# Optimization experiments

Hardware: AMD Instinct MI355X
Metric: run time of the kernel (lower is better)

## Reference

```python
import jax, jax.numpy as jnp
import numpy as np

N_HEADS = 16
EMBED_DIM = 2048
BATCH, SEQ = 2, 2048


def setup_inputs() -> dict:
    key = jax.random.key(0)
    k1, k2, k3, k4, k5 = jax.random.split(key, 5)
    s_in = 1.0 / np.sqrt(EMBED_DIM)
    return {
        "x": jax.random.normal(k1, (BATCH, SEQ, EMBED_DIM), dtype=jnp.float32),
        "w_in": jax.random.normal(k2, (3 * EMBED_DIM, EMBED_DIM), dtype=jnp.float32) * s_in,
        "b_in": jax.random.normal(k3, (3 * EMBED_DIM,), dtype=jnp.float32) * 0.02,
        "w_out": jax.random.normal(k4, (EMBED_DIM, EMBED_DIM), dtype=jnp.float32) * s_in,
        "b_out": jax.random.normal(k5, (EMBED_DIM,), dtype=jnp.float32) * 0.02,
        "causal_mask": 1,
    }


def reference(x, w_in, b_in, w_out, b_out, causal_mask):
    b, l, e = x.shape
    h, d = N_HEADS, e // N_HEADS
    qkv = x @ w_in.T + b_in                      # [b, l, 3e]
    q, k, v = jnp.split(qkv, 3, axis=-1)
    # b l (h d) -> b h l d
    q = q.reshape(b, l, h, d).transpose(0, 2, 1, 3)
    k = k.reshape(b, l, h, d).transpose(0, 2, 1, 3)
    v = v.reshape(b, l, h, d).transpose(0, 2, 1, 3)
    scores = jnp.einsum("bhqd,bhkd->bhqk", q, k) / jnp.sqrt(jnp.float32(d))
    if causal_mask:
        tri = jnp.triu(jnp.ones((l, l), dtype=bool), k=1)  # True above diagonal
        scores = jnp.where(tri, -jnp.inf, scores)
    attn = jax.nn.softmax(scores, axis=-1)
    out = jnp.einsum("bhqk,bhkd->bhqd", attn, v)  # [b, h, l, d]
    out = out.transpose(0, 2, 1, 3).reshape(b, l, e)
    return out @ w_out.T + b_out
```

## Files before the change

### kernel.cpp

```cpp
#include <hip/hip_runtime.h>
#include <hip/hip_bf16.h>
#include <math.h>

typedef __attribute__((ext_vector_type(4))) float floatx4;
typedef __attribute__((ext_vector_type(16))) float floatx16;
typedef __attribute__((ext_vector_type(8))) __bf16 bf16x8;

__device__ __forceinline__ unsigned short f2bf(float f) {
    union { float f; unsigned int u; } v; v.f = f;
    unsigned int u = v.u;
    u += 0x7FFFu + ((u >> 16) & 1u);
    return (unsigned short)(u >> 16);
}

__device__ __forceinline__ unsigned int pkbf(float a, float b) {
    return (unsigned int)f2bf(a) | ((unsigned int)f2bf(b) << 16);
}

__device__ __forceinline__ void gl_lds16(const void* g, void* l) {
    __builtin_amdgcn_global_load_lds(
        (const __attribute__((address_space(1))) void*)g,
        (__attribute__((address_space(3))) void*)l, 16, 0, 0);
}

__global__ void cast_f32_bf16(const float* __restrict__ in,
                              unsigned short* __restrict__ out, int n) {
    int i = (blockIdx.x * blockDim.x + threadIdx.x) * 4;
    if (i + 4 <= n) {
        float4 f = *(const float4*)(in + i);
        ushort4 o;
        o.x = f2bf(f.x); o.y = f2bf(f.y); o.z = f2bf(f.z); o.w = f2bf(f.w);
        *(ushort4*)(out + i) = o;
    }
}

#define BM 128
#define BN 128
#define BK 32
#define GROUP_M 8

template<int MODE>
__global__ __launch_bounds__(256) void gemm_nt(
    const unsigned short* __restrict__ A,
    const unsigned short* __restrict__ B,
    const float* __restrict__ bias,
    float* __restrict__ Cf,
    unsigned short* __restrict__ q_ws,
    unsigned short* __restrict__ k_ws,
    unsigned short* __restrict__ vT_ws,
    int M, int N, int K)
{
    __shared__ unsigned short Asm[BM][BK];
    __shared__ unsigned short Bsm[BN][BK];

    const int id = blockIdx.x + gridDim.x * blockIdx.y;
    const int perGroup = gridDim.x * GROUP_M;
    const int group = id / perGroup;
    const int rem = id % perGroup;
    const int gh = min(GROUP_M, (int)gridDim.y - group * GROUP_M);
    const int by = group * GROUP_M + rem % gh;
    const int bx = rem / gh;

    const int m0 = by * BM, n0 = bx * BN;
    const int tid = threadIdx.x;
    const int lane = tid & 63, wid = tid >> 6;
    const int quad = lane >> 4, li = lane & 15;
    const int wy = wid >> 1, wx = wid & 1;

    const int lrow = lane >> 2;
    const int lcol = (lane & 3) * 8;

    floatx4 acc[4][4] = {};

    const int kTiles = K / BK;
    for (int kt = 0; kt < kTiles; ++kt) {
        const int k0 = kt * BK;
        #pragma unroll
        for (int c = 0; c < 2; ++c) {
            const int cidx = wid * 2 + c;
            const int row = cidx * 16 + lrow;
            gl_lds16(A + (size_t)(m0 + row) * K + k0 + lcol,
                     &Asm[0][0] + cidx * 512);
            gl_lds16(B + (size_t)(n0 + row) * K + k0 + lcol,
                     &Bsm[0][0] + cidx * 512);
        }
        __syncthreads();

        bf16x8 af[4], bfr[4];
        #pragma unroll
        for (int t = 0; t < 4; ++t) {
            af[t]  = *(const bf16x8*)(&Asm[wy * 64 + t * 16 + li][quad * 8]);
            bfr[t] = *(const bf16x8*)(&Bsm[wx * 64 + t * 16 + li][quad * 8]);
        }
        #pragma unroll
        for (int i = 0; i < 4; ++i)
            #pragma unroll
            for (int j = 0; j < 4; ++j)
                acc[i][j] = __builtin_amdgcn_mfma_f32_16x16x32_bf16(
                    af[i], bfr[j], acc[i][j], 0, 0, 0);
        __syncthreads();
    }

    if (MODE == 0) {
        #pragma unroll
        for (int i = 0; i < 4; ++i)
            #pragma unroll
            for (int j = 0; j < 4; ++j) {
                int col = wx * 64 + j * 16 + li;
                float bv = bias[n0 + col];
                #pragma unroll
                for (int r = 0; r < 4; ++r) {
                    int row = wy * 64 + i * 16 + quad * 4 + r;
                    Cf[(size_t)(m0 + row) * N + n0 + col] = acc[i][j][r] + bv;
                }
            }
    } else {
        const int which = bx >> 4;
        const int h = bx & 15;
        const int b = by >> 4;
        const int lbase = (by & 15) * BM;
        const size_t bh = (size_t)(b * 16 + h);
        #pragma unroll
        for (int i = 0; i < 4; ++i)
            #pragma unroll
            for (int j = 0; j < 4; ++j) {
                int col = wx * 64 + j * 16 + li;
                float bv = bias[n0 + col];
                #pragma unroll
                for (int r = 0; r < 4; ++r) {
                    int row = wy * 64 + i * 16 + quad * 4 + r;
                    int l = lbase + row;
                    unsigned short ob = f2bf(acc[i][j][r] + bv);
                    if (which == 0)      q_ws[(bh * 2048 + l) * 128 + col] = ob;
                    else if (which == 1) k_ws[(bh * 2048 + l) * 128 + col] = ob;
                    else                 vT_ws[(bh * 128 + col) * 2048 + l] = ob;
                }
            }
    }
}

#define AP 8
__global__ __launch_bounds__(256, 2) void attn_kernel(
    const unsigned short* __restrict__ q_ws,
    const unsigned short* __restrict__ k_ws,
    const unsigned short* __restrict__ vT_ws,
    unsigned short* __restrict__ aout,
    const int* __restrict__ causal_ptr)
{
    __shared__ unsigned short Ksm[128][128 + AP];
    __shared__ unsigned short Vsm[128][128 + AP];

    const int ord = blockIdx.x;
    int qt, bhid;
    if (ord < 256) { qt = ord >> 5;              bhid = ord & 31; }
    else           { qt = 15 - ((ord - 256) >> 5); bhid = ord & 31; }
    const int b = bhid >> 4, h = bhid & 15;

    const int tid = threadIdx.x;
    const int lane = tid & 63, w = tid >> 6;
    const int lq = lane & 31;
    const int half = lane >> 5;
    const size_t bh = (size_t)(b * 16 + h);
    const unsigned short* Qp = q_ws + bh * 2048 * 128;
    const unsigned short* Kp = k_ws + bh * 2048 * 128;
    const unsigned short* Vp = vT_ws + bh * 128 * 2048;
    const int causal = causal_ptr[0];
    const float scale = 0.08838834764831845f;

    const int qg = qt * 128 + w * 32 + lq;
    bf16x8 qf[8];
    #pragma unroll
    for (int s = 0; s < 8; ++s)
        qf[s] = *(const bf16x8*)(Qp + (size_t)qg * 128 + s * 16 + half * 8);

    floatx16 O[4] = {};
    float m_i = -INFINITY, l_i = 0.f;

    const int myEnd = causal ? qt : 15;
    for (int kt = 0; kt <= myEnd; ++kt) {
        #pragma unroll
        for (int c = 0; c < 8; ++c) {
            int chunk = c * 256 + tid;
            int row = chunk >> 4;
            int cc  = (chunk & 15) * 8;
            *(uint4*)(&Ksm[row][cc]) =
                *(const uint4*)(Kp + (size_t)(kt * 128 + row) * 128 + cc);
            *(uint4*)(&Vsm[row][cc]) =
                *(const uint4*)(Vp + (size_t)row * 2048 + kt * 128 + cc);
        }
        __syncthreads();

        floatx16 S[4] = {};
        #pragma unroll
        for (int ct = 0; ct < 4; ++ct)
            #pragma unroll
            for (int s = 0; s < 8; ++s) {
                bf16x8 kf = *(const bf16x8*)(&Ksm[ct * 32 + lq][s * 16 + half * 8]);
                S[ct] = __builtin_amdgcn_mfma_f32_32x32x16_bf16(kf, qf[s], S[ct], 0, 0, 0);
            }

        const bool diag = causal && (kt == qt);
        float mx = -INFINITY;
        #pragma unroll
        for (int ct = 0; ct < 4; ++ct)
            #pragma unroll
            for (int r = 0; r < 16; ++r) {
                float sv = S[ct][r] * scale;
                if (diag) {
                    int key = 32 * ct + (r & 3) + 8 * (r >> 2) + 4 * half;
                    if (kt * 128 + key > qg) sv = -INFINITY;
                }
                S[ct][r] = sv;
                mx = fmaxf(mx, sv);
            }
        mx = fmaxf(mx, __shfl_xor(mx, 32, 64));
        float m_new = fmaxf(m_i, mx);
        float m_use = (m_new == -INFINITY) ? 0.f : m_new;
        float alpha = __expf(m_i - m_use);

        float rs = 0.f;
        #pragma unroll
        for (int ct = 0; ct < 4; ++ct)
            #pragma unroll
            for (int r = 0; r < 16; ++r) {
                float p = __expf(S[ct][r] - m_use);
                S[ct][r] = p;
                rs += p;
            }
        rs += __shfl_xor(rs, 32, 64);
        l_i = l_i * alpha + rs;
        m_i = m_new;
        #pragma unroll
        for (int dt = 0; dt < 4; ++dt)
            #pragma unroll
            for (int r = 0; r < 16; ++r)
                O[dt][r] *= alpha;

        bf16x8 pfr[8];
        #pragma unroll
        for (int ct = 0; ct < 4; ++ct)
            #pragma unroll
            for (int h2 = 0; h2 < 2; ++h2) {
                int base = 8 * h2;
                unsigned int pk0 = pkbf(S[ct][base + 0], S[ct][base + 1]);
                unsigned int pk1 = pkbf(S[ct][base + 2], S[ct][base + 3]);
                unsigned int pk2 = pkbf(S[ct][base + 4], S[ct][base + 5]);
                unsigned int pk3 = pkbf(S[ct][base + 6], S[ct][base + 7]);
                unsigned int x0 = __shfl_xor((int)pk0, 32, 64);
                unsigned int x1 = __shfl_xor((int)pk1, 32, 64);
                unsigned int x2 = __shfl_xor((int)pk2, 32, 64);
                unsigned int x3 = __shfl_xor((int)pk3, 32, 64);
                union { unsigned int u[4]; bf16x8 v; } fr;
                fr.u[0] = half ? x2 : pk0;
                fr.u[1] = half ? x3 : pk1;
                fr.u[2] = half ? pk2 : x0;
                fr.u[3] = half ? pk3 : x1;
                pfr[ct * 2 + h2] = fr.v;
            }

        #pragma unroll
        for (int dt = 0; dt < 4; ++dt)
            #pragma unroll
            for (int s = 0; s < 8; ++s) {
                bf16x8 vf = *(const bf16x8*)(&Vsm[dt * 32 + lq][s * 16 + half * 8]);
                O[dt] = __builtin_amdgcn_mfma_f32_32x32x16_bf16(vf, pfr[s], O[dt], 0, 0, 0);
            }
        __syncthreads();
    }

    const float invl = 1.0f / l_i;
    #pragma unroll
    for (int dt = 0; dt < 4; ++dt)
        #pragma unroll
        for (int g = 0; g < 4; ++g) {
            int dbase = dt * 32 + g * 8 + half * 4;
            ushort4 o4;
            o4.x = f2bf(O[dt][g * 4 + 0] * invl);
            o4.y = f2bf(O[dt][g * 4 + 1] * invl);
            o4.z = f2bf(O[dt][g * 4 + 2] * invl);
            o4.w = f2bf(O[dt][g * 4 + 3] * invl);
            *(ushort4*)(&Ksm[w * 32 + lq][dbase]) = o4;
        }
    __syncthreads();
    #pragma unroll
    for (int c = 0; c < 8; ++c) {
        int chunk = c * 256 + tid;
        int row = chunk >> 4;
        int dc = (chunk & 15) * 8;
        uint4 v = *(const uint4*)(&Ksm[row][dc]);
        *(uint4*)(aout + ((size_t)b * 2048 + qt * 128 + row) * 2048 + h * 128 + dc) = v;
    }
}

extern "C" void kernel_launch(void* const* d_in, const int* in_sizes, int n_in,
                              void* d_out, int out_size, void* d_ws, size_t ws_size,
                              hipStream_t stream) {
    const float* x     = (const float*)d_in[0];
    const float* w_in  = (const float*)d_in[1];
    const float* b_in  = (const float*)d_in[2];
    const float* w_out = (const float*)d_in[3];
    const float* b_out = (const float*)d_in[4];
    const int* causal  = (const int*)d_in[5];

    char* ws = (char*)d_ws;
    unsigned short* xb    = (unsigned short*)ws; ws += (size_t)4096 * 2048 * 2;
    unsigned short* wb    = (unsigned short*)ws; ws += (size_t)6144 * 2048 * 2;
    unsigned short* wob   = (unsigned short*)ws; ws += (size_t)2048 * 2048 * 2;
    unsigned short* q_ws  = (unsigned short*)ws; ws += (size_t)32 * 2048 * 128 * 2;
    unsigned short* k_ws  = (unsigned short*)ws; ws += (size_t)32 * 2048 * 128 * 2;
    unsigned short* vT_ws = (unsigned short*)ws; ws += (size_t)32 * 2048 * 128 * 2;
    unsigned short* aout  = (unsigned short*)ws; ws += (size_t)4096 * 2048 * 2;

    cast_f32_bf16<<<8192, 256, 0, stream>>>(x, xb, 4096 * 2048);
    cast_f32_bf16<<<12288, 256, 0, stream>>>(w_in, wb, 6144 * 2048);
    cast_f32_bf16<<<4096, 256, 0, stream>>>(w_out, wob, 2048 * 2048);

    gemm_nt<1><<<dim3(48, 32), 256, 0, stream>>>(
        xb, wb, b_in, nullptr, q_ws, k_ws, vT_ws, 4096, 6144, 2048);

    attn_kernel<<<512, 256, 0, stream>>>(
        q_ws, k_ws, vT_ws, aout, causal);

    gemm_nt<0><<<dim3(16, 32), 256, 0, stream>>>(
        aout, wob, b_out, (float*)d_out, nullptr, nullptr, nullptr,
        4096, 2048, 2048);
}
```

Baseline: 434.4 us.

## Replace GEMM with 256x256 double-buffered 8-wave pipelined kernel with swizzled LDS

Replaces the simple 128x128x32 GEMM, which synchronized on every K step, with a 256x256 tile, BK=64 kernel using 512 threads. It double-buffers A/B tiles in 128KB of dynamic LDS, issues global->LDS loads interleaved with MFMA phases, and waits on explicit vmcnt counts. LDS addresses are XOR-swizzled to avoid bank conflicts, MFMA blocks are raised with setprio, and workgroups are remapped across XCDs. The V-transpose store is vectorized to ushort4. This adds complexity and tight manual synchronization. The output projection launches only 128 workgroups, which may underfill the GPU.

```diff
diff --git a/kernel.cpp b/kernel.cpp
--- a/kernel.cpp
+++ b/kernel.cpp
@@ -34,13 +34,43 @@
     }
 }
 
-#define BM 128
-#define BN 128
-#define BK 32
-#define GROUP_M 8
+
+#define VMCNT(n) asm volatile("s_waitcnt vmcnt(" #n ")" ::: "memory")
+#define BARF()   do { __builtin_amdgcn_s_barrier(); asm volatile("" ::: "memory"); } while (0)
+
+#define STAGE_A(bsel, tt, h) do { \
+    const unsigned short* _s = Ab + (size_t)((h) * 128 + rstage) * K + (tt) * 64 + scol; \
+    char* _d = bufc + (bsel) * 65536 + (h) * 16384 + wid * 1024; \
+    gl_lds16(_s, _d); \
+    gl_lds16(_s + (size_t)64 * K, _d + 8192); \
+} while (0)
+
+#define STAGE_B(bsel, tt, h) do { \
+    const unsigned short* _s = Bb + (size_t)((h) * 128 + rstage) * K + (tt) * 64 + scol; \
+    char* _d = bufc + (bsel) * 65536 + 32768 + (h) * 16384 + wid * 1024; \
+    gl_lds16(_s, _d); \
+    gl_lds16(_s + (size_t)64 * K, _d + 8192); \
+} while (0)
+
+#define RDA(base, ii, kse) (*(const bf16x8*)((base) + (ii) * 2048 + rdoffA + (kse)))
+#define RDB(base, jj, kse) (*(const bf16x8*)((base) + (jj) * 2048 + rdoffB + (kse)))
+
+#define MFMA_Q(iofs, jofs, BV) do { \
+    __builtin_amdgcn_s_setprio(1); \
+    _Pragma("unroll") \
+    for (int ii = 0; ii < 4; ++ii) { \
+        _Pragma("unroll") \
+        for (int jj = 0; jj < 2; ++jj) { \
+            acc[(iofs) + ii][(jofs) + jj] = __builtin_amdgcn_mfma_f32_16x16x32_bf16( \
+                aF[ii * 2 + 0], BV[jj * 2 + 0], acc[(iofs) + ii][(jofs) + jj], 0, 0, 0); \
+            acc[(iofs) + ii][(jofs) + jj] = __builtin_amdgcn_mfma_f32_16x16x32_bf16( \
+                aF[ii * 2 + 1], BV[jj * 2 + 1], acc[(iofs) + ii][(jofs) + jj], 0, 0, 0); \
+        } } \
+    __builtin_amdgcn_s_setprio(0); \
+} while (0)
 
 template<int MODE>
-__global__ __launch_bounds__(256) void gemm_nt(
+__global__ __launch_bounds__(512, 2) void gemm8p(
     const unsigned short* __restrict__ A,
     const unsigned short* __restrict__ B,
     const float* __restrict__ bias,
@@ -50,90 +80,146 @@
     unsigned short* __restrict__ vT_ws,
     int M, int N, int K)
 {
-    __shared__ unsigned short Asm[BM][BK];
-    __shared__ unsigned short Bsm[BN][BK];
-
-    const int id = blockIdx.x + gridDim.x * blockIdx.y;
-    const int perGroup = gridDim.x * GROUP_M;
-    const int group = id / perGroup;
-    const int rem = id % perGroup;
-    const int gh = min(GROUP_M, (int)gridDim.y - group * GROUP_M);
-    const int by = group * GROUP_M + rem % gh;
-    const int bx = rem / gh;
-
-    const int m0 = by * BM, n0 = bx * BN;
+    extern __shared__ char ldsc[];
+    char* const bufc = ldsc;
+
+    const int nby = M >> 8;
+    const int nwg = gridDim.x;
+    const int qq = nwg >> 3;
+    const int wg = (blockIdx.x & 7) * qq + (blockIdx.x >> 3);
+    const int by = wg % nby, bx = wg / nby;
+    const int m0 = by << 8, n0 = bx << 8;
+
     const int tid = threadIdx.x;
     const int lane = tid & 63, wid = tid >> 6;
-    const int quad = lane >> 4, li = lane & 15;
-    const int wy = wid >> 1, wx = wid & 1;
-
-    const int lrow = lane >> 2;
-    const int lcol = (lane & 3) * 8;
-
-    floatx4 acc[4][4] = {};
-
-    const int kTiles = K / BK;
-    for (int kt = 0; kt < kTiles; ++kt) {
-        const int k0 = kt * BK;
-        #pragma unroll
-        for (int c = 0; c < 2; ++c) {
-            const int cidx = wid * 2 + c;
-            const int row = cidx * 16 + lrow;
-            gl_lds16(A + (size_t)(m0 + row) * K + k0 + lcol,
-                     &Asm[0][0] + cidx * 512);
-            gl_lds16(B + (size_t)(n0 + row) * K + k0 + lcol,
-                     &Bsm[0][0] + cidx * 512);
-        }
-        __syncthreads();
-
-        bf16x8 af[4], bfr[4];
-        #pragma unroll
-        for (int t = 0; t < 4; ++t) {
-            af[t]  = *(const bf16x8*)(&Asm[wy * 64 + t * 16 + li][quad * 8]);
-            bfr[t] = *(const bf16x8*)(&Bsm[wx * 64 + t * 16 + li][quad * 8]);
-        }
-        #pragma unroll
-        for (int i = 0; i < 4; ++i)
-            #pragma unroll
-            for (int j = 0; j < 4; ++j)
-                acc[i][j] = __builtin_amdgcn_mfma_f32_16x16x32_bf16(
-                    af[i], bfr[j], acc[i][j], 0, 0, 0);
-        __syncthreads();
+    const int li = lane & 15, quad = lane >> 4;
+    const int wr = wid >> 2, wc = wid & 3;
+
+    const int rstage = tid >> 3;
+    const int scol = (((tid & 7) ^ ((tid >> 3) & 7)) << 3);
+    const unsigned short* Ab = A + (size_t)m0 * K;
+    const unsigned short* Bb = B + (size_t)n0 * K;
+
+    const int swz = (lane & 7) << 4;
+    const int ks0 = ((quad << 4)     ) ^ swz;
+    const int ks1 = ((quad << 4) + 64) ^ swz;
+    const int rdoffA = li * 128;
+    const int rdoffB = li * 128 + ((wc & 1) << 13);
+
+    const char* rdA0 = bufc + wr * 16384;
+    const char* rdB0 = bufc + 32768 + (wc >> 1) * 16384;
+    const char* rdA1 = rdA0 + 65536;
+    const char* rdB1 = rdB0 + 65536;
+
+    floatx4 acc[8][4] = {};
+    bf16x8 aF[8], bL[4], bH[4];
+
+    const int KTn = K >> 6;
+
+    STAGE_A(0, 0, 0); STAGE_A(0, 0, 1); STAGE_B(0, 0, 0); STAGE_B(0, 0, 1);
+    STAGE_B(1, 1, 0); STAGE_B(1, 1, 1); STAGE_A(1, 1, 0);
+    VMCNT(6);
+    BARF();
+
+    for (int t = 0; t < KTn; t += 2) {
+        const bool pf = (t + 2 < KTn);
+
+        #pragma unroll
+        for (int ii = 0; ii < 4; ++ii) { aF[ii*2+0] = RDA(rdA0, ii, ks0); aF[ii*2+1] = RDA(rdA0, ii, ks1); }
+        #pragma unroll
+        for (int jj = 0; jj < 2; ++jj) { bL[jj*2+0] = RDB(rdB0, jj, ks0); bL[jj*2+1] = RDB(rdB0, jj, ks1); }
+        STAGE_A(1, t + 1, 1);
+        BARF();
+        MFMA_Q(0, 0, bL);
+        BARF();
+
+        #pragma unroll
+        for (int jj = 0; jj < 2; ++jj) { bH[jj*2+0] = RDB(rdB0, 2 + jj, ks0); bH[jj*2+1] = RDB(rdB0, 2 + jj, ks1); }
+        BARF();
+        MFMA_Q(0, 2, bH);
+        BARF();
+
+        #pragma unroll
+        for (int ii = 0; ii < 4; ++ii) { aF[ii*2+0] = RDA(rdA0, 4 + ii, ks0); aF[ii*2+1] = RDA(rdA0, 4 + ii, ks1); }
+        if (pf) STAGE_B(0, t + 2, 0);
+        BARF();
+        MFMA_Q(4, 0, bL);
+        BARF();
+
+        if (pf) { STAGE_B(0, t + 2, 1); STAGE_A(0, t + 2, 0); }
+        BARF();
+        MFMA_Q(4, 2, bH);
+        if (pf) { VMCNT(6); } else { VMCNT(0); }
+        BARF();
+
+        #pragma unroll
+        for (int ii = 0; ii < 4; ++ii) { aF[ii*2+0] = RDA(rdA1, ii, ks0); aF[ii*2+1] = RDA(rdA1, ii, ks1); }
+        #pragma unroll
+        for (int jj = 0; jj < 2; ++jj) { bL[jj*2+0] = RDB(rdB1, jj, ks0); bL[jj*2+1] = RDB(rdB1, jj, ks1); }
+        if (pf) STAGE_A(0, t + 2, 1);
+        BARF();
+        MFMA_Q(0, 0, bL);
+        BARF();
+
+        #pragma unroll
+        for (int jj = 0; jj < 2; ++jj) { bH[jj*2+0] = RDB(rdB1, 2 + jj, ks0); bH[jj*2+1] = RDB(rdB1, 2 + jj, ks1); }
+        BARF();
+        MFMA_Q(0, 2, bH);
+        BARF();
+
+        #pragma unroll
+        for (int ii = 0; ii < 4; ++ii) { aF[ii*2+0] = RDA(rdA1, 4 + ii, ks0); aF[ii*2+1] = RDA(rdA1, 4 + ii, ks1); }
+        if (pf) STAGE_B(1, t + 3, 0);
+        BARF();
+        MFMA_Q(4, 0, bL);
+        BARF();
+
+        if (pf) { STAGE_B(1, t + 3, 1); STAGE_A(1, t + 3, 0); }
+        BARF();
+        MFMA_Q(4, 2, bH);
+        VMCNT(6);
+        BARF();
     }
 
+    const int colb = n0 + wc * 64;
+    const int rowb = m0 + wr * 128;
     if (MODE == 0) {
         #pragma unroll
-        for (int i = 0; i < 4; ++i)
-            #pragma unroll
-            for (int j = 0; j < 4; ++j) {
-                int col = wx * 64 + j * 16 + li;
-                float bv = bias[n0 + col];
+        for (int i2 = 0; i2 < 8; ++i2)
+            #pragma unroll
+            for (int j2 = 0; j2 < 4; ++j2) {
+                const int col = colb + j2 * 16 + li;
+                const float bv = bias[col];
                 #pragma unroll
                 for (int r = 0; r < 4; ++r) {
-                    int row = wy * 64 + i * 16 + quad * 4 + r;
-                    Cf[(size_t)(m0 + row) * N + n0 + col] = acc[i][j][r] + bv;
+                    const int row = rowb + i2 * 16 + quad * 4 + r;
+                    Cf[(size_t)row * N + col] = acc[i2][j2][r] + bv;
                 }
             }
     } else {
-        const int which = bx >> 4;
-        const int h = bx & 15;
-        const int b = by >> 4;
-        const int lbase = (by & 15) * BM;
-        const size_t bh = (size_t)(b * 16 + h);
-        #pragma unroll
-        for (int i = 0; i < 4; ++i)
-            #pragma unroll
-            for (int j = 0; j < 4; ++j) {
-                int col = wx * 64 + j * 16 + li;
-                float bv = bias[n0 + col];
-                #pragma unroll
-                for (int r = 0; r < 4; ++r) {
-                    int row = wy * 64 + i * 16 + quad * 4 + r;
-                    int l = lbase + row;
-                    unsigned short ob = f2bf(acc[i][j][r] + bv);
-                    if (which == 0)      q_ws[(bh * 2048 + l) * 128 + col] = ob;
-                    else if (which == 1) k_ws[(bh * 2048 + l) * 128 + col] = ob;
-                    else                 vT_ws[(bh * 128 + col) * 2048 + l] = ob;
+        const int bb = m0 >> 11;
+        const int which = n0 >> 11;
+        #pragma unroll
+        for (int i2 = 0; i2 < 8; ++i2)
+            #pragma unroll
+            for (int j2 = 0; j2 < 4; ++j2) {
+                const int ng = colb + j2 * 16 + li;
+                const float bv = bias[ng];
+                const int e = ng & 2047, hh = e >> 7, dd = e & 127;
+                const size_t bh = (size_t)(bb * 16 + hh);
+                const int l0 = (rowb + i2 * 16 + quad * 4) & 2047;
+                if (which == 2) {
+                    ushort4 o4;
+                    o4.x = f2bf(acc[i2][j2][0] + bv);
+                    o4.y = f2bf(acc[i2][j2][1] + bv);
+                    o4.z = f2bf(acc[i2][j2][2] + bv);
+                    o4.w = f2bf(acc[i2][j2][3] + bv);
+                    *(ushort4*)(vT_ws + (bh * 128 + dd) * 2048 + l0) = o4;
+                } else {
+                    unsigned short* dst = (which == 0) ? q_ws : k_ws;
+                    #pragma unroll
+                    for (int r = 0; r < 4; ++r)
+                        dst[(bh * 2048 + (l0 + r)) * 128 + dd] = f2bf(acc[i2][j2][r] + bv);
                 }
             }
     }
@@ -311,17 +397,28 @@
     unsigned short* vT_ws = (unsigned short*)ws; ws += (size_t)32 * 2048 * 128 * 2;
     unsigned short* aout  = (unsigned short*)ws; ws += (size_t)4096 * 2048 * 2;
 
+    static int once = []() {
+        auto* f0 = gemm8p<0>;
+        auto* f1 = gemm8p<1>;
+        hipFuncSetAttribute((const void*)f0,
+            hipFuncAttributeMaxDynamicSharedMemorySize, 131072);
+        hipFuncSetAttribute((const void*)f1,
+            hipFuncAttributeMaxDynamicSharedMemorySize, 131072);
+        return 0;
+    }();
+    (void)once;
+
     cast_f32_bf16<<<8192, 256, 0, stream>>>(x, xb, 4096 * 2048);
     cast_f32_bf16<<<12288, 256, 0, stream>>>(w_in, wb, 6144 * 2048);
     cast_f32_bf16<<<4096, 256, 0, stream>>>(w_out, wob, 2048 * 2048);
 
-    gemm_nt<1><<<dim3(48, 32), 256, 0, stream>>>(
+    gemm8p<1><<<384, 512, 131072, stream>>>(
         xb, wb, b_in, nullptr, q_ws, k_ws, vT_ws, 4096, 6144, 2048);
 
     attn_kernel<<<512, 256, 0, stream>>>(
         q_ws, k_ws, vT_ws, aout, causal);
 
-    gemm_nt<0><<<dim3(16, 32), 256, 0, stream>>>(
+    gemm8p<0><<<128, 512, 131072, stream>>>(
         aout, wob, b_out, (float*)d_out, nullptr, nullptr, nullptr,
         4096, 2048, 2048);
 }
```

Result: faster. 394.4 us (-9.2%).
